# Kernel tuning notes

Hardware: AMD Instinct MI355X
Metric: run time of the kernel (lower is better)

Reference implementation:

```python
import jax, jax.numpy as jnp
import numpy as np

B, T, C = 4, 2048, 1024
H, D = 16, 64  # num_heads, head_dim
P = 64         # prefix length


def setup_inputs() -> dict:
    key = jax.random.key(0)
    ks = jax.random.split(key, 12)
    s = 1.0 / np.sqrt(C)
    return {
        "x": jax.random.normal(ks[0], (B, T, C), dtype=jnp.float32),
        "attn_mask": jax.random.randint(ks[1], (B, 1, 1, T), 0, 2, dtype=jnp.int32),
        "prefix_k": jax.random.normal(ks[2], (B, H, P, D), dtype=jnp.float32),
        "prefix_v": jax.random.normal(ks[3], (B, H, P, D), dtype=jnp.float32),
        "Wq": jax.random.normal(ks[4], (C, C), dtype=jnp.float32) * s,
        "bq": jnp.zeros((C,), dtype=jnp.float32),
        "Wk": jax.random.normal(ks[5], (C, C), dtype=jnp.float32) * s,
        "bk": jnp.zeros((C,), dtype=jnp.float32),
        "Wv": jax.random.normal(ks[6], (C, C), dtype=jnp.float32) * s,
        "bv": jnp.zeros((C,), dtype=jnp.float32),
        "Wo": jax.random.normal(ks[7], (C, C), dtype=jnp.float32) * s,
        "bo": jnp.zeros((C,), dtype=jnp.float32),
    }


def _heads(y):
    # [B,T,C] -> [B,H,T,D]
    return y.reshape(B, T, H, D).transpose(0, 2, 1, 3)


def reference(x, attn_mask, prefix_k, prefix_v, Wq, bq, Wk, bk, Wv, bv, Wo, bo):
    q = _heads(x @ Wq.T + bq)
    k = _heads(x @ Wk.T + bk)
    v = _heads(x @ Wv.T + bv)
    # concat prefix K/V along key dim -> [B,H,P+T,D]
    k = jnp.concatenate([prefix_k, k], axis=2)
    v = jnp.concatenate([prefix_v, v], axis=2)
    # prefix positions are always visible
    prefix_mask = jnp.ones((B, 1, 1, P), dtype=attn_mask.dtype)
    mask = jnp.concatenate([prefix_mask, attn_mask], axis=-1)  # [B,1,1,P+T]
    scores = jnp.einsum('bhtd,bhsd->bhts', q, k) / jnp.sqrt(jnp.asarray(D, x.dtype))
    scores = jnp.where(mask == 0, -jnp.inf, scores)
    w = jax.nn.softmax(scores, axis=-1)
    o = jnp.einsum('bhts,bhsd->bhtd', w, v)
    o = o.transpose(0, 2, 1, 3).reshape(B, T, C)
    return o @ Wo.T + bo
```

## Files before the change

kernel.cpp:

```cpp
#include <hip/hip_runtime.h>
#include <hip/hip_bf16.h>

typedef __bf16 bf16;
typedef __attribute__((ext_vector_type(8))) __bf16 bf16x8;
typedef __attribute__((ext_vector_type(4))) __bf16 bf16x4;
typedef __attribute__((ext_vector_type(4))) float f32x4;
typedef __attribute__((ext_vector_type(16))) float f32x16;

#define MFMA16(a, b, c) __builtin_amdgcn_mfma_f32_16x16x32_bf16(a, b, c, 0, 0, 0)
#define MFMA32(a, b, c) __builtin_amdgcn_mfma_f32_32x32x16_bf16(a, b, c, 0, 0, 0)

__device__ __forceinline__ void gl_lds16(const void* g, void* l) {
    __builtin_amdgcn_global_load_lds(
        (const __attribute__((address_space(1))) void*)g,
        (__attribute__((address_space(3))) void*)l, 16, 0, 0);
}

#define BARRIER() do { asm volatile("" ::: "memory"); \
    __builtin_amdgcn_s_barrier(); asm volatile("" ::: "memory"); } while (0)

#define QSCALE 0.18033688011f
#define LOGBIAS 24.0f

__device__ __forceinline__ int vsig4(int c) {
    return ((c >> 4) << 4) + (((c >> 3) & 1) << 2) + ((c & 4) ? 8 : 0);
}

__global__ __launch_bounds__(256) void prep(
    const float* __restrict__ x, const float* __restrict__ Wq,
    const float* __restrict__ Wk, const float* __restrict__ Wv,
    const float* __restrict__ Wo, const float* __restrict__ pk,
    const float* __restrict__ pv, const int* __restrict__ mask,
    bf16* __restrict__ xb, bf16* __restrict__ wb,
    bf16* __restrict__ k_ws, bf16* __restrict__ vt_ws,
    int* __restrict__ ridx, int* __restrict__ nkv)
{
    const int blk = blockIdx.x, tid = threadIdx.x;
    if (blk < 4) {
        const int b = blk, lane = tid & 63, wv = tid >> 6;
        const int* mb = mask + b * 2048;
        int loc[8], s = 0;
#pragma unroll
        for (int e = 0; e < 8; ++e) { loc[e] = (mb[tid * 8 + e] != 0); s += loc[e]; }
        int inc = s;
#pragma unroll
        for (int off = 1; off < 64; off <<= 1) {
            int t = __shfl_up(inc, off);
            if (lane >= off) inc += t;
        }
        __shared__ int wt[4];
        if (lane == 63) wt[wv] = inc;
        __syncthreads();
        int wo = 0;
        for (int w = 0; w < wv; ++w) wo += wt[w];
        int excl = wo + inc - s;
#pragma unroll
        for (int e = 0; e < 8; ++e) {
            if (loc[e]) ridx[b * 2048 + excl] = tid * 8 + e;
            excl += loc[e];
        }
        if (tid == 255) nkv[b] = 64 + wo + inc;
    } else if (blk < 260) {
        int i = (blk - 4) * 256 + tid;
        {
            int base = i * 4;
            int bh = base >> 12, rem = base & 4095;
            float4 a = *(const float4*)&pk[base];
            bf16x4 ab;
            ab[0] = (bf16)a.x; ab[1] = (bf16)a.y; ab[2] = (bf16)a.z; ab[3] = (bf16)a.w;
            *(bf16x4*)&k_ws[(size_t)bh * (2112 * 64) + rem] = ab;
        }
        {
            int bh = i >> 10, r = i & 1023;
            int d = r >> 4, sq = (r & 15) * 4;
            bf16x4 vb;
#pragma unroll
            for (int e = 0; e < 4; ++e)
                vb[e] = (bf16)pv[(size_t)bh * 4096 + (sq + e) * 64 + d];
            *(bf16x4*)&vt_ws[((size_t)bh * 64 + d) * 2112 + vsig4(sq)] = vb;
        }
    } else {
        int i8 = (blk - 260) * 256 + tid;
        const float* src; bf16* dst; size_t off;
        if (i8 < 1048576) { src = x; dst = xb; off = (size_t)i8; }
        else {
            int j = i8 - 1048576;
            int sel = j >> 17;
            off = (size_t)(j & 131071);
            src = (sel == 0) ? Wq : (sel == 1) ? Wk : (sel == 2) ? Wv : Wo;
            dst = wb + (size_t)sel * 1048576;
        }
        float4 a = *(const float4*)&src[off * 8];
        float4 c = *(const float4*)&src[off * 8 + 4];
        bf16x8 o;
        o[0] = (bf16)a.x; o[1] = (bf16)a.y; o[2] = (bf16)a.z; o[3] = (bf16)a.w;
        o[4] = (bf16)c.x; o[5] = (bf16)c.y; o[6] = (bf16)c.z; o[7] = (bf16)c.w;
        *(bf16x8*)&dst[off * 8] = o;
    }
}

__device__ __forceinline__ void gemm_tile128(
    const bf16* a0, const bf16* a1, const bf16* a2, const bf16* a3,
    const bf16* b0, const bf16* b1, const bf16* b2, const bf16* b3,
    bf16* lds, const int wave, const int lane, f32x4 (&acc)[4][4])
{
    const int ln = lane & 15, quad = lane >> 4;
    const int wm = wave >> 1, wn = wave & 1;
    const int soA = wave * 512;
    const int c0 = (quad * 8) ^ ((ln & 7) << 3);
    const int c1 = (32 + quad * 8) ^ ((ln & 7) << 3);
    const int aBase = (wm * 64 + ln) * 64;
    const int bBase = 8192 + (wn * 64 + ln) * 64;

    gl_lds16(a0, lds + soA);
    gl_lds16(a1, lds + 2048 + soA);
    gl_lds16(a2, lds + 4096 + soA);
    gl_lds16(a3, lds + 6144 + soA);
    gl_lds16(b0, lds + 8192 + soA);
    gl_lds16(b1, lds + 10240 + soA);
    gl_lds16(b2, lds + 12288 + soA);
    gl_lds16(b3, lds + 14336 + soA);
    gl_lds16(a0 + 64, lds + 16384 + soA);
    gl_lds16(a1 + 64, lds + 16384 + 2048 + soA);
    gl_lds16(a2 + 64, lds + 16384 + 4096 + soA);
    gl_lds16(a3 + 64, lds + 16384 + 6144 + soA);

#pragma unroll 2
    for (int t = 0; t < 16; ++t) {
        bf16* cur = lds + ((t & 1) ? 16384 : 0);
        bf16* nxt = lds + ((t & 1) ? 0 : 16384);

        if (t < 15) asm volatile("s_waitcnt vmcnt(4)" ::: "memory");
        else        asm volatile("s_waitcnt vmcnt(0)" ::: "memory");
        BARRIER();

        bf16x8 fa[4][2], fb[4][2];
#pragma unroll
        for (int mi = 0; mi < 4; ++mi) {
            fa[mi][0] = *(const bf16x8*)(cur + aBase + mi * 1024 + c0);
            fa[mi][1] = *(const bf16x8*)(cur + aBase + mi * 1024 + c1);
        }
#pragma unroll
        for (int ni = 0; ni < 4; ++ni) {
            fb[ni][0] = *(const bf16x8*)(cur + bBase + ni * 1024 + c0);
            fb[ni][1] = *(const bf16x8*)(cur + bBase + ni * 1024 + c1);
        }
        if (t < 15) {
            const int kn = (t + 1) * 64;
            gl_lds16(b0 + kn, nxt + 8192 + soA);
            gl_lds16(b1 + kn, nxt + 10240 + soA);
            gl_lds16(b2 + kn, nxt + 12288 + soA);
            gl_lds16(b3 + kn, nxt + 14336 + soA);
        }
        __builtin_amdgcn_s_setprio(1);
#pragma unroll
        for (int mi = 0; mi < 4; ++mi)
#pragma unroll
            for (int ni = 0; ni < 4; ++ni) {
                acc[mi][ni] = MFMA16(fa[mi][0], fb[ni][0], acc[mi][ni]);
                acc[mi][ni] = MFMA16(fa[mi][1], fb[ni][1], acc[mi][ni]);
            }
        __builtin_amdgcn_s_setprio(0);
        BARRIER();
        if (t < 14) {
            const int kn = (t + 2) * 64;
            gl_lds16(a0 + kn, cur + soA);
            gl_lds16(a1 + kn, cur + 2048 + soA);
            gl_lds16(a2 + kn, cur + 4096 + soA);
            gl_lds16(a3 + kn, cur + 6144 + soA);
        }
    }
}

__global__ __launch_bounds__(256, 2) void proj_gemm(
    const bf16* __restrict__ X, const bf16* __restrict__ Wb,
    const float* __restrict__ bq, const float* __restrict__ bk,
    const float* __restrict__ bv, const int* __restrict__ ridx,
    const int* __restrict__ nkv,
    bf16* __restrict__ q_ws, bf16* __restrict__ k_ws, bf16* __restrict__ vt_ws)
{
    __shared__ bf16 lds[32768];
    const int hw = blockIdx.x;
    const int bx = (hw & 7) * 192 + (hw >> 3);
    const int tid = threadIdx.x, wave = tid >> 6, lane = tid & 63;
    const int sr = tid >> 3;
    const int csw = ((tid & 7) ^ (sr & 7)) << 3;

    int kind, m0 = 0, bsel = 0, nvis = 0, mbase = 0, n0;
    const bf16* W;
    const float* bias;
    if (bx < 512) {
        kind = 0; m0 = (bx >> 3) * 128; n0 = (bx & 7) * 128;
        W = Wb; bias = bq;
    } else {
        int j = bx - 512;
        kind = 1 + (j >> 9);
        int r = j & 511;
        bsel = r >> 7;
        int rr = r & 127;
        mbase = (rr >> 3) * 128;
        n0 = (rr & 7) * 128;
        nvis = nkv[bsel] - 64;
        if (mbase >= nvis) return;
        W = Wb + (size_t)kind * 1048576;
        bias = (kind == 1) ? bk : bv;
    }

    const bf16 *a0, *a1, *a2, *a3;
    if (kind == 0) {
        a0 = X + (size_t)(m0 + sr) * 1024 + csw;
        a1 = a0 + (size_t)32 * 1024;
        a2 = a0 + (size_t)64 * 1024;
        a3 = a0 + (size_t)96 * 1024;
    } else {
        const int* rb = ridx + bsel * 2048;
        const int nv1 = nvis - 1;
        int g = mbase + sr;
        int e0 = (g      < nv1) ? g      : nv1;
        int e1 = (g + 32 < nv1) ? g + 32 : nv1;
        int e2 = (g + 64 < nv1) ? g + 64 : nv1;
        int e3 = (g + 96 < nv1) ? g + 96 : nv1;
        const bf16* Xb = X + (size_t)bsel * 2048 * 1024 + csw;
        a0 = Xb + (size_t)rb[e0] * 1024;
        a1 = Xb + (size_t)rb[e1] * 1024;
        a2 = Xb + (size_t)rb[e2] * 1024;
        a3 = Xb + (size_t)rb[e3] * 1024;
    }
    const bf16* b0 = W + (size_t)(n0 + sr) * 1024 + csw;
    const bf16* b1 = b0 + (size_t)32 * 1024;
    const bf16* b2 = b0 + (size_t)64 * 1024;
    const bf16* b3 = b0 + (size_t)96 * 1024;

    const f32x4 z4 = {0.f, 0.f, 0.f, 0.f};
    f32x4 acc[4][4];
#pragma unroll
    for (int i = 0; i < 4; ++i)
#pragma unroll
        for (int j = 0; j < 4; ++j) acc[i][j] = z4;

    gemm_tile128(a0, a1, a2, a3, b0, b1, b2, b3, lds, wave, lane, acc);

    const int ln = lane & 15, quad = lane >> 4;
    const int wm = wave >> 1, wn = wave & 1;
    if (kind == 0) {
#pragma unroll
        for (int ni = 0; ni < 4; ++ni) {
            const int n = n0 + wn * 64 + ni * 16 + ln;
            const float bb = bias[n];
            const int h = n >> 6, d = n & 63;
#pragma unroll
            for (int mi = 0; mi < 4; ++mi) {
                int m = m0 + wm * 64 + mi * 16 + quad * 4;
                int b = m >> 11, tq = m & 2047;
#pragma unroll
                for (int r = 0; r < 4; ++r)
                    q_ws[((size_t)(b * 16 + h) * 2048 + tq + r) * 64 + d] =
                        (bf16)((acc[mi][ni][r] + bb) * QSCALE);
            }
        }
    } else {
#pragma unroll
        for (int ni = 0; ni < 4; ++ni) {
            const int n = n0 + wn * 64 + ni * 16 + ln;
            const float bb = bias[n];
            const int h = n >> 6, d = n & 63;
            const size_t bh64 = (size_t)(bsel * 16 + h);
#pragma unroll
            for (int mi = 0; mi < 4; ++mi) {
                int ml = mbase + wm * 64 + mi * 16 + quad * 4;
                if (kind == 1) {
#pragma unroll
                    for (int r = 0; r < 4; ++r)
                        if (ml + r < nvis)
                            k_ws[(bh64 * 2112 + 64 + ml + r) * 64 + d] =
                                (bf16)(acc[mi][ni][r] + bb);
                } else {
                    int g0 = 64 + ml;
                    int c0v = g0 & 63;
                    int gcol = (g0 & ~63) + vsig4(c0v);
                    if (ml + 3 < nvis) {
                        bf16x4 pb;
#pragma unroll
                        for (int r = 0; r < 4; ++r) pb[r] = (bf16)(acc[mi][ni][r] + bb);
                        *(bf16x4*)&vt_ws[(bh64 * 64 + d) * 2112 + gcol] = pb;
                    } else {
#pragma unroll
                        for (int r = 0; r < 4; ++r)
                            if (ml + r < nvis)
                                vt_ws[(bh64 * 64 + d) * 2112 + gcol + r] =
                                    (bf16)(acc[mi][ni][r] + bb);
                    }
                }
            }
        }
    }
}

__global__ __launch_bounds__(256, 2) void attn_kernel(
    const bf16* __restrict__ Q, const bf16* __restrict__ K,
    const bf16* __restrict__ VT, const int* __restrict__ nk,
    bf16* __restrict__ O)
{
    __shared__ bf16 smem[128 * 72];
    bf16* Ks = smem;
    bf16* Vt = smem + 64 * 72;
    const int tid = threadIdx.x, wave = tid >> 6, lane = tid & 63;
    const int ln = lane & 31, hh = lane >> 5;
    const int hw = blockIdx.x;
    const int bh = (hw & 7) * 8 + ((hw >> 3) & 7);
    const int qx = hw >> 6;
    const int b = bh >> 4, head = bh & 15;
    const bf16* __restrict__ Kb  = K  + (size_t)bh * (2112 * 64);
    const bf16* __restrict__ Vtb = VT + (size_t)bh * (64 * 2112);
    const int nkeys = nk[b];
    const int send = ((nkeys + 63) >> 6) << 6;
    const int qg = qx * 256 + wave * 64 + ln;

    bf16x8 qf0[4], qf1[4];
#pragma unroll
    for (int kt = 0; kt < 4; ++kt) {
        qf0[kt] = *(const bf16x8*)&Q[((size_t)bh * 2048 + qg) * 64 + kt * 16 + hh * 8];
        qf1[kt] = *(const bf16x8*)&Q[((size_t)bh * 2048 + qg + 32) * 64 + kt * 16 + hh * 8];
    }

    f32x16 m24;
#pragma unroll
    for (int r = 0; r < 16; ++r) m24[r] = -LOGBIAS;

    float l0 = 0.f, l1 = 0.f;
    f32x16 acc00, acc01, acc10, acc11;
#pragma unroll
    for (int r = 0; r < 16; ++r) {
        acc00[r] = 0.f; acc01[r] = 0.f; acc10[r] = 0.f; acc11[r] = 0.f;
    }

    const int ks_s = tid >> 3, ks_c = (tid & 7) * 8;
    const int vd = tid >> 3, vs = (tid & 7) * 8;

    bf16x8 kr0, kr1, vr0, vr1;
    kr0 = *(const bf16x8*)&Kb[(size_t)ks_s * 64 + ks_c];
    kr1 = *(const bf16x8*)&Kb[(size_t)(ks_s + 32) * 64 + ks_c];
    vr0 = *(const bf16x8*)&Vtb[(size_t)vd * 2112 + vs];
    vr1 = *(const bf16x8*)&Vtb[(size_t)(vd + 32) * 2112 + vs];

    for (int s0 = 0; s0 < send; s0 += 64) {
        __syncthreads();
        *(bf16x8*)&Ks[ks_s * 72 + ks_c]        = kr0;
        *(bf16x8*)&Ks[(ks_s + 32) * 72 + ks_c] = kr1;
        *(bf16x8*)&Vt[vd * 72 + vs]            = vr0;
        *(bf16x8*)&Vt[(vd + 32) * 72 + vs]     = vr1;
        __syncthreads();

        if (s0 + 64 < send) {
            const int sn = s0 + 64;
            kr0 = *(const bf16x8*)&Kb[(size_t)(sn + ks_s) * 64 + ks_c];
            kr1 = *(const bf16x8*)&Kb[(size_t)(sn + ks_s + 32) * 64 + ks_c];
            vr0 = *(const bf16x8*)&Vtb[(size_t)vd * 2112 + sn + vs];
            vr1 = *(const bf16x8*)&Vtb[(size_t)(vd + 32) * 2112 + sn + vs];
        }

        f32x16 sc0[2], sc1[2];
        __builtin_amdgcn_s_setprio(1);
#pragma unroll
        for (int ts = 0; ts < 2; ++ts) {
            bf16x8 kf = *(const bf16x8*)&Ks[(ts * 32 + ln) * 72 + hh * 8];
            f32x16 sA = MFMA32(kf, qf0[0], m24);
            f32x16 sB = MFMA32(kf, qf1[0], m24);
#pragma unroll
            for (int kt = 1; kt < 4; ++kt) {
                kf = *(const bf16x8*)&Ks[(ts * 32 + ln) * 72 + kt * 16 + hh * 8];
                sA = MFMA32(kf, qf0[kt], sA);
                sB = MFMA32(kf, qf1[kt], sB);
            }
            sc0[ts] = sA; sc1[ts] = sB;
        }
        __builtin_amdgcn_s_setprio(0);

        float rs0 = 0.f, rs1 = 0.f;
        bf16x8 pf0[4], pf1[4];
        if (s0 + 64 <= nkeys) {
#pragma unroll
            for (int ts = 0; ts < 2; ++ts)
#pragma unroll
                for (int rg = 0; rg < 4; ++rg)
#pragma unroll
                    for (int i = 0; i < 4; ++i) {
                        float p0 = __builtin_amdgcn_exp2f(sc0[ts][rg * 4 + i]);
                        float p1 = __builtin_amdgcn_exp2f(sc1[ts][rg * 4 + i]);
                        rs0 += p0; rs1 += p1;
                        pf0[ts * 2 + (rg >> 1)][(rg & 1) * 4 + i] = (bf16)p0;
                        pf1[ts * 2 + (rg >> 1)][(rg & 1) * 4 + i] = (bf16)p1;
                    }
        } else {
#pragma unroll
            for (int ts = 0; ts < 2; ++ts)
#pragma unroll
                for (int rg = 0; rg < 4; ++rg)
#pragma unroll
                    for (int i = 0; i < 4; ++i) {
                        int key = s0 + ts * 32 + rg * 8 + hh * 4 + i;
                        float add = (key < nkeys) ? 0.f : -1e30f;
                        float p0 = __builtin_amdgcn_exp2f(sc0[ts][rg * 4 + i] + add);
                        float p1 = __builtin_amdgcn_exp2f(sc1[ts][rg * 4 + i] + add);
                        rs0 += p0; rs1 += p1;
                        pf0[ts * 2 + (rg >> 1)][(rg & 1) * 4 + i] = (bf16)p0;
                        pf1[ts * 2 + (rg >> 1)][(rg & 1) * 4 + i] = (bf16)p1;
                    }
        }
        l0 += rs0; l1 += rs1;

        __builtin_amdgcn_s_setprio(1);
#pragma unroll
        for (int st = 0; st < 4; ++st) {
            bf16x8 a0 = *(const bf16x8*)&Vt[ln * 72 + st * 16 + hh * 8];
            acc00 = MFMA32(a0, pf0[st], acc00);
            acc10 = MFMA32(a0, pf1[st], acc10);
            bf16x8 a1 = *(const bf16x8*)&Vt[(32 + ln) * 72 + st * 16 + hh * 8];
            acc01 = MFMA32(a1, pf0[st], acc01);
            acc11 = MFMA32(a1, pf1[st], acc11);
        }
        __builtin_amdgcn_s_setprio(0);
    }

    __syncthreads();
    l0 += __shfl_xor(l0, 32);
    l1 += __shfl_xor(l1, 32);
    const float inv0 = 1.0f / l0, inv1 = 1.0f / l1;
    bf16* scratch = smem + wave * (32 * 72);
    const int orow = lane >> 3, oc = (lane & 7) * 8;
    const int qrow0 = qx * 256 + wave * 64;

#pragma unroll
    for (int rg = 0; rg < 4; ++rg) {
        bf16x4 ob;
#pragma unroll
        for (int i = 0; i < 4; ++i) ob[i] = (bf16)(acc00[rg * 4 + i] * inv0);
        *(bf16x4*)&scratch[ln * 72 + rg * 8 + hh * 4] = ob;
#pragma unroll
        for (int i = 0; i < 4; ++i) ob[i] = (bf16)(acc01[rg * 4 + i] * inv0);
        *(bf16x4*)&scratch[ln * 72 + 32 + rg * 8 + hh * 4] = ob;
    }
    __builtin_amdgcn_s_waitcnt(0xC07F);
    __builtin_amdgcn_sched_barrier(0);
#pragma unroll
    for (int pass = 0; pass < 4; ++pass) {
        int ml = pass * 8 + orow;
        bf16x8 ov = *(const bf16x8*)&scratch[ml * 72 + oc];
        *(bf16x8*)&O[((size_t)b * 2048 + qrow0 + ml) * 1024 + head * 64 + oc] = ov;
    }
    __builtin_amdgcn_s_waitcnt(0xC07F);
    __builtin_amdgcn_sched_barrier(0);

#pragma unroll
    for (int rg = 0; rg < 4; ++rg) {
        bf16x4 ob;
#pragma unroll
        for (int i = 0; i < 4; ++i) ob[i] = (bf16)(acc10[rg * 4 + i] * inv1);
        *(bf16x4*)&scratch[ln * 72 + rg * 8 + hh * 4] = ob;
#pragma unroll
        for (int i = 0; i < 4; ++i) ob[i] = (bf16)(acc11[rg * 4 + i] * inv1);
        *(bf16x4*)&scratch[ln * 72 + 32 + rg * 8 + hh * 4] = ob;
    }
    __builtin_amdgcn_s_waitcnt(0xC07F);
    __builtin_amdgcn_sched_barrier(0);
#pragma unroll
    for (int pass = 0; pass < 4; ++pass) {
        int ml = pass * 8 + orow;
        bf16x8 ov = *(const bf16x8*)&scratch[ml * 72 + oc];
        *(bf16x8*)&O[((size_t)b * 2048 + qrow0 + 32 + ml) * 1024 + head * 64 + oc] = ov;
    }
}

__global__ __launch_bounds__(256, 2) void out_proj_gemm(
    const bf16* __restrict__ A, const bf16* __restrict__ W,
    const float* __restrict__ bias, float* __restrict__ out)
{
    __shared__ bf16 lds[32768];
    const int hw = blockIdx.x;
    const int bx = (hw & 7) * 64 + (hw >> 3);
    const int m0 = (bx >> 3) * 128, n0 = (bx & 7) * 128;
    const int tid = threadIdx.x, wave = tid >> 6, lane = tid & 63;
    const int sr = tid >> 3;
    const int csw = ((tid & 7) ^ (sr & 7)) << 3;

    const bf16* a0 = A + (size_t)(m0 + sr) * 1024 + csw;
    const bf16* a1 = a0 + (size_t)32 * 1024;
    const bf16* a2 = a0 + (size_t)64 * 1024;
    const bf16* a3 = a0 + (size_t)96 * 1024;
    const bf16* b0 = W + (size_t)(n0 + sr) * 1024 + csw;
    const bf16* b1 = b0 + (size_t)32 * 1024;
    const bf16* b2 = b0 + (size_t)64 * 1024;
    const bf16* b3 = b0 + (size_t)96 * 1024;

    const f32x4 z4 = {0.f, 0.f, 0.f, 0.f};
    f32x4 acc[4][4];
#pragma unroll
    for (int i = 0; i < 4; ++i)
#pragma unroll
        for (int j = 0; j < 4; ++j) acc[i][j] = z4;

    gemm_tile128(a0, a1, a2, a3, b0, b1, b2, b3, lds, wave, lane, acc);

    const int ln = lane & 15, quad = lane >> 4;
    const int wm = wave >> 1, wn = wave & 1;
#pragma unroll
    for (int ni = 0; ni < 4; ++ni) {
        const int n = n0 + wn * 64 + ni * 16 + ln;
        const float bb = bias[n];
#pragma unroll
        for (int mi = 0; mi < 4; ++mi) {
            int m = m0 + wm * 64 + mi * 16 + quad * 4;
#pragma unroll
            for (int r = 0; r < 4; ++r)
                out[(size_t)(m + r) * 1024 + n] = acc[mi][ni][r] + bb;
        }
    }
}

extern "C" void kernel_launch(void* const* d_in, const int* in_sizes, int n_in,
                              void* d_out, int out_size, void* d_ws, size_t ws_size,
                              hipStream_t stream)
{
    const float* x    = (const float*)d_in[0];
    const int*   mask = (const int*)d_in[1];
    const float* pk   = (const float*)d_in[2];
    const float* pv   = (const float*)d_in[3];
    const float* Wq   = (const float*)d_in[4];
    const float* bq   = (const float*)d_in[5];
    const float* Wk   = (const float*)d_in[6];
    const float* bk   = (const float*)d_in[7];
    const float* Wv   = (const float*)d_in[8];
    const float* bv   = (const float*)d_in[9];
    const float* Wo   = (const float*)d_in[10];
    const float* bo   = (const float*)d_in[11];
    float* out = (float*)d_out;

    bf16* xb    = (bf16*)d_ws;
    bf16* wb    = xb + (size_t)8388608;
    bf16* q_ws  = wb + (size_t)4194304;
    bf16* k_ws  = q_ws + (size_t)8388608;
    bf16* vt_ws = k_ws + (size_t)8650752;
    int*  ridx  = (int*)(vt_ws + (size_t)8650752);
    int*  nkv   = ridx + 4 * 2048;
    bf16* a_ws  = xb;

    prep<<<dim3(6404), 256, 0, stream>>>(x, Wq, Wk, Wv, Wo, pk, pv, mask,
                                         xb, wb, k_ws, vt_ws, ridx, nkv);
    proj_gemm<<<dim3(1536), 256, 0, stream>>>(xb, wb, bq, bk, bv, ridx, nkv,
                                              q_ws, k_ws, vt_ws);
    attn_kernel<<<dim3(512), 256, 0, stream>>>(q_ws, k_ws, vt_ws, nkv, a_ws);
    out_proj_gemm<<<dim3(512), 256, 0, stream>>>(a_ws, wb + (size_t)3 * 1048576,
                                                 bo, out);
}
```

Baseline: 234.2 us.

## Rewrite projection GEMM with BK=32 double-buffered tiles and higher occupancy

The QKV projection GEMM now uses a new main loop with a K-step of 32 and two 8K-element LDS buffers instead of a K-step of 64, halving shared memory per block so the launch bound can rise from 2 to 4 blocks per CU. Block-to-tile mapping is interleaved so Q, K and V tiles alternate (kind = bx % 3), with a new ordering of M tiles for K/V, to balance the early-exit work across CUs. The loads use a new XOR swizzle suited to 32-wide rows. In exchange there are twice as many loop iterations and barriers per tile, and less data reuse per barrier.

```diff
diff --git a/kernel.cpp b/kernel.cpp
--- a/kernel.cpp
+++ b/kernel.cpp
@@ -96,6 +96,172 @@
         o[0] = (bf16)a.x; o[1] = (bf16)a.y; o[2] = (bf16)a.z; o[3] = (bf16)a.w;
         o[4] = (bf16)c.x; o[5] = (bf16)c.y; o[6] = (bf16)c.z; o[7] = (bf16)c.w;
         *(bf16x8*)&dst[off * 8] = o;
+    }
+}
+
+__device__ __forceinline__ void gemm_bk32(
+    const bf16* a0, const bf16* a1, const bf16* b0, const bf16* b1,
+    bf16* lds, const int wave, const int lane, f32x4 (&acc)[4][4])
+{
+    const int ln = lane & 15, quad = lane >> 4;
+    const int wm = wave >> 1, wn = wave & 1;
+    const int so = wave * 512;
+    const int rc = (quad ^ ((ln >> 1) & 3)) << 3;
+    const int aBase = (wm * 64 + ln) * 32;
+    const int bBase = 4096 + (wn * 64 + ln) * 32;
+
+#define BUF32(u) (((u) & 1) * 8192)
+#define STG32(u) do { const int kn_ = (u) * 32; \
+    gl_lds16(a0 + kn_, lds + BUF32(u) + so); \
+    gl_lds16(a1 + kn_, lds + BUF32(u) + 2048 + so); \
+    gl_lds16(b0 + kn_, lds + BUF32(u) + 4096 + so); \
+    gl_lds16(b1 + kn_, lds + BUF32(u) + 6144 + so); } while (0)
+
+    STG32(0);
+#pragma unroll 2
+    for (int t = 0; t < 32; ++t) {
+        const bf16* cur = lds + BUF32(t);
+        if (t < 31) {
+            STG32(t + 1);
+            asm volatile("s_waitcnt vmcnt(4)" ::: "memory");
+        } else {
+            asm volatile("s_waitcnt vmcnt(0)" ::: "memory");
+        }
+        BARRIER();
+
+        bf16x8 fa[4], fb[4];
+#pragma unroll
+        for (int mi = 0; mi < 4; ++mi)
+            fa[mi] = *(const bf16x8*)(cur + aBase + mi * 512 + rc);
+#pragma unroll
+        for (int ni = 0; ni < 4; ++ni)
+            fb[ni] = *(const bf16x8*)(cur + bBase + ni * 512 + rc);
+        __builtin_amdgcn_s_setprio(1);
+#pragma unroll
+        for (int mi = 0; mi < 4; ++mi)
+#pragma unroll
+            for (int ni = 0; ni < 4; ++ni)
+                acc[mi][ni] = MFMA16(fa[mi], fb[ni], acc[mi][ni]);
+        __builtin_amdgcn_s_setprio(0);
+        BARRIER();
+    }
+#undef BUF32
+#undef STG32
+}
+
+__global__ __launch_bounds__(256, 4) void proj_gemm(
+    const bf16* __restrict__ X, const bf16* __restrict__ Wb,
+    const float* __restrict__ bq, const float* __restrict__ bk,
+    const float* __restrict__ bv, const int* __restrict__ ridx,
+    const int* __restrict__ nkv,
+    bf16* __restrict__ q_ws, bf16* __restrict__ k_ws, bf16* __restrict__ vt_ws)
+{
+    __shared__ bf16 lds[16384];
+    const int hw = blockIdx.x;
+    const int bx = (hw & 7) * 192 + (hw >> 3);
+    const int kind = bx % 3;
+    const int idx = bx / 3;
+    const int tid = threadIdx.x, wave = tid >> 6, lane = tid & 63;
+    const int sr = tid >> 2;
+    const int csw = (((tid & 3) ^ ((tid >> 3) & 3)) << 3);
+
+    int m0 = 0, bsel = 0, nvis = 0, mbase = 0, n0;
+    const bf16* W;
+    const float* bias;
+    if (kind == 0) {
+        m0 = (idx >> 3) * 128; n0 = (idx & 7) * 128;
+        W = Wb; bias = bq;
+    } else {
+        int p = idx >> 5;
+        int mt = ((p & 1) << 3) | (p >> 1);
+        bsel = (idx >> 3) & 3;
+        n0 = (idx & 7) * 128;
+        mbase = mt * 128;
+        nvis = nkv[bsel] - 64;
+        if (mbase >= nvis) return;
+        W = Wb + (size_t)kind * 1048576;
+        bias = (kind == 1) ? bk : bv;
+    }
+
+    const bf16 *a0, *a1;
+    if (kind == 0) {
+        a0 = X + (size_t)(m0 + sr) * 1024 + csw;
+        a1 = a0 + (size_t)64 * 1024;
+    } else {
+        const int* rb = ridx + bsel * 2048;
+        const int nv1 = nvis - 1;
+        int g = mbase + sr;
+        int e0 = (g      < nv1) ? g      : nv1;
+        int e1 = (g + 64 < nv1) ? g + 64 : nv1;
+        const bf16* Xb = X + (size_t)bsel * 2048 * 1024 + csw;
+        a0 = Xb + (size_t)rb[e0] * 1024;
+        a1 = Xb + (size_t)rb[e1] * 1024;
+    }
+    const bf16* b0 = W + (size_t)(n0 + sr) * 1024 + csw;
+    const bf16* b1 = b0 + (size_t)64 * 1024;
+
+    const f32x4 z4 = {0.f, 0.f, 0.f, 0.f};
+    f32x4 acc[4][4];
+#pragma unroll
+    for (int i = 0; i < 4; ++i)
+#pragma unroll
+        for (int j = 0; j < 4; ++j) acc[i][j] = z4;
+
+    gemm_bk32(a0, a1, b0, b1, lds, wave, lane, acc);
+
+    const int ln = lane & 15, quad = lane >> 4;
+    const int wm = wave >> 1, wn = wave & 1;
+    if (kind == 0) {
+#pragma unroll
+        for (int ni = 0; ni < 4; ++ni) {
+            const int n = n0 + wn * 64 + ni * 16 + ln;
+            const float bb = bias[n];
+            const int h = n >> 6, d = n & 63;
+#pragma unroll
+            for (int mi = 0; mi < 4; ++mi) {
+                int m = m0 + wm * 64 + mi * 16 + quad * 4;
+                int b = m >> 11, tq = m & 2047;
+#pragma unroll
+                for (int r = 0; r < 4; ++r)
+                    q_ws[((size_t)(b * 16 + h) * 2048 + tq + r) * 64 + d] =
+                        (bf16)((acc[mi][ni][r] + bb) * QSCALE);
+            }
+        }
+    } else {
+#pragma unroll
+        for (int ni = 0; ni < 4; ++ni) {
+            const int n = n0 + wn * 64 + ni * 16 + ln;
+            const float bb = bias[n];
+            const int h = n >> 6, d = n & 63;
+            const size_t bh64 = (size_t)(bsel * 16 + h);
+#pragma unroll
+            for (int mi = 0; mi < 4; ++mi) {
+                int ml = mbase + wm * 64 + mi * 16 + quad * 4;
+                if (kind == 1) {
+#pragma unroll
+                    for (int r = 0; r < 4; ++r)
+                        if (ml + r < nvis)
+                            k_ws[(bh64 * 2112 + 64 + ml + r) * 64 + d] =
+                                (bf16)(acc[mi][ni][r] + bb);
+                } else {
+                    int g0 = 64 + ml;
+                    int c0v = g0 & 63;
+                    int gcol = (g0 & ~63) + vsig4(c0v);
+                    if (ml + 3 < nvis) {
+                        bf16x4 pb;
+#pragma unroll
+                        for (int r = 0; r < 4; ++r) pb[r] = (bf16)(acc[mi][ni][r] + bb);
+                        *(bf16x4*)&vt_ws[(bh64 * 64 + d) * 2112 + gcol] = pb;
+                    } else {
+#pragma unroll
+                        for (int r = 0; r < 4; ++r)
+                            if (ml + r < nvis)
+                                vt_ws[(bh64 * 64 + d) * 2112 + gcol + r] =
+                                    (bf16)(acc[mi][ni][r] + bb);
+                    }
+                }
+            }
+        }
     }
 }
 
@@ -168,130 +334,6 @@
             gl_lds16(a1 + kn, cur + 2048 + soA);
             gl_lds16(a2 + kn, cur + 4096 + soA);
             gl_lds16(a3 + kn, cur + 6144 + soA);
-        }
-    }
-}
-
-__global__ __launch_bounds__(256, 2) void proj_gemm(
-    const bf16* __restrict__ X, const bf16* __restrict__ Wb,
-    const float* __restrict__ bq, const float* __restrict__ bk,
-    const float* __restrict__ bv, const int* __restrict__ ridx,
-    const int* __restrict__ nkv,
-    bf16* __restrict__ q_ws, bf16* __restrict__ k_ws, bf16* __restrict__ vt_ws)
-{
-    __shared__ bf16 lds[32768];
-    const int hw = blockIdx.x;
-    const int bx = (hw & 7) * 192 + (hw >> 3);
-    const int tid = threadIdx.x, wave = tid >> 6, lane = tid & 63;
-    const int sr = tid >> 3;
-    const int csw = ((tid & 7) ^ (sr & 7)) << 3;
-
-    int kind, m0 = 0, bsel = 0, nvis = 0, mbase = 0, n0;
-    const bf16* W;
-    const float* bias;
-    if (bx < 512) {
-        kind = 0; m0 = (bx >> 3) * 128; n0 = (bx & 7) * 128;
-        W = Wb; bias = bq;
-    } else {
-        int j = bx - 512;
-        kind = 1 + (j >> 9);
-        int r = j & 511;
-        bsel = r >> 7;
-        int rr = r & 127;
-        mbase = (rr >> 3) * 128;
-        n0 = (rr & 7) * 128;
-        nvis = nkv[bsel] - 64;
-        if (mbase >= nvis) return;
-        W = Wb + (size_t)kind * 1048576;
-        bias = (kind == 1) ? bk : bv;
-    }
-
-    const bf16 *a0, *a1, *a2, *a3;
-    if (kind == 0) {
-        a0 = X + (size_t)(m0 + sr) * 1024 + csw;
-        a1 = a0 + (size_t)32 * 1024;
-        a2 = a0 + (size_t)64 * 1024;
-        a3 = a0 + (size_t)96 * 1024;
-    } else {
-        const int* rb = ridx + bsel * 2048;
-        const int nv1 = nvis - 1;
-        int g = mbase + sr;
-        int e0 = (g      < nv1) ? g      : nv1;
-        int e1 = (g + 32 < nv1) ? g + 32 : nv1;
-        int e2 = (g + 64 < nv1) ? g + 64 : nv1;
-        int e3 = (g + 96 < nv1) ? g + 96 : nv1;
-        const bf16* Xb = X + (size_t)bsel * 2048 * 1024 + csw;
-        a0 = Xb + (size_t)rb[e0] * 1024;
-        a1 = Xb + (size_t)rb[e1] * 1024;
-        a2 = Xb + (size_t)rb[e2] * 1024;
-        a3 = Xb + (size_t)rb[e3] * 1024;
-    }
-    const bf16* b0 = W + (size_t)(n0 + sr) * 1024 + csw;
-    const bf16* b1 = b0 + (size_t)32 * 1024;
-    const bf16* b2 = b0 + (size_t)64 * 1024;
-    const bf16* b3 = b0 + (size_t)96 * 1024;
-
-    const f32x4 z4 = {0.f, 0.f, 0.f, 0.f};
-    f32x4 acc[4][4];
-#pragma unroll
-    for (int i = 0; i < 4; ++i)
-#pragma unroll
-        for (int j = 0; j < 4; ++j) acc[i][j] = z4;
-
-    gemm_tile128(a0, a1, a2, a3, b0, b1, b2, b3, lds, wave, lane, acc);
-
-    const int ln = lane & 15, quad = lane >> 4;
-    const int wm = wave >> 1, wn = wave & 1;
-    if (kind == 0) {
-#pragma unroll
-        for (int ni = 0; ni < 4; ++ni) {
-            const int n = n0 + wn * 64 + ni * 16 + ln;
-            const float bb = bias[n];
-            const int h = n >> 6, d = n & 63;
-#pragma unroll
-            for (int mi = 0; mi < 4; ++mi) {
-                int m = m0 + wm * 64 + mi * 16 + quad * 4;
-                int b = m >> 11, tq = m & 2047;
-#pragma unroll
-                for (int r = 0; r < 4; ++r)
-                    q_ws[((size_t)(b * 16 + h) * 2048 + tq + r) * 64 + d] =
-                        (bf16)((acc[mi][ni][r] + bb) * QSCALE);
-            }
-        }
-    } else {
-#pragma unroll
-        for (int ni = 0; ni < 4; ++ni) {
-            const int n = n0 + wn * 64 + ni * 16 + ln;
-            const float bb = bias[n];
-            const int h = n >> 6, d = n & 63;
-            const size_t bh64 = (size_t)(bsel * 16 + h);
-#pragma unroll
-            for (int mi = 0; mi < 4; ++mi) {
-                int ml = mbase + wm * 64 + mi * 16 + quad * 4;
-                if (kind == 1) {
-#pragma unroll
-                    for (int r = 0; r < 4; ++r)
-                        if (ml + r < nvis)
-                            k_ws[(bh64 * 2112 + 64 + ml + r) * 64 + d] =
-                                (bf16)(acc[mi][ni][r] + bb);
-                } else {
-                    int g0 = 64 + ml;
-                    int c0v = g0 & 63;
-                    int gcol = (g0 & ~63) + vsig4(c0v);
-                    if (ml + 3 < nvis) {
-                        bf16x4 pb;
-#pragma unroll
-                        for (int r = 0; r < 4; ++r) pb[r] = (bf16)(acc[mi][ni][r] + bb);
-                        *(bf16x4*)&vt_ws[(bh64 * 64 + d) * 2112 + gcol] = pb;
-                    } else {
-#pragma unroll
-                        for (int r = 0; r < 4; ++r)
-                            if (ml + r < nvis)
-                                vt_ws[(bh64 * 64 + d) * 2112 + gcol + r] =
-                                    (bf16)(acc[mi][ni][r] + bb);
-                    }
-                }
-            }
         }
     }
 }
```

New measurement: 233.7 us. Within noise of the previous version (-0.2%).
